# Kernel tuning notes

Hardware: AMD Instinct MI355X
Metric: run time of the kernel (lower is better)

The kernel has to match this reference:

```python
import jax, jax.numpy as jnp
import numpy as np

N = 16384      # nodes
E = 524288     # edges (avg degree 32)
D = 128        # node_dim
H = 256        # hidden_dim
C = 10         # num_classes
G = 64         # graphs in batch


def setup_inputs() -> dict:
    key = jax.random.key(0)
    ks = jax.random.split(key, 8)
    x = jax.random.normal(ks[0], (N, D), dtype=jnp.float32)
    edge_index = jax.random.randint(ks[1], (2, E), 0, N)
    batch = jnp.sort(jax.random.randint(ks[2], (N,), 0, G))
    s = 0.05
    W1 = jax.random.normal(ks[3], (D, H), dtype=jnp.float32) * s
    b1 = jnp.zeros((H,), dtype=jnp.float32)
    W2 = jax.random.normal(ks[4], (H, H), dtype=jnp.float32) * s
    b2 = jnp.zeros((H,), dtype=jnp.float32)
    Wc = jax.random.normal(ks[5], (H, C), dtype=jnp.float32) * s
    bc = jnp.zeros((C,), dtype=jnp.float32)
    return {"x": x, "edge_index": edge_index, "batch": batch,
            "W1": W1, "b1": b1, "W2": W2, "b2": b2, "Wc": Wc, "bc": bc}


def _adj_norm(edge_index, n, dtype):
    # dense adjacency with self-loops (duplicates collapse to 1 via .set),
    # symmetric degree normalization D^{-1/2} A D^{-1/2}
    adj = jnp.zeros((n, n), dtype=dtype)
    adj = adj.at[edge_index[0], edge_index[1]].set(1.0)
    diag = jnp.arange(n)
    adj = adj.at[diag, diag].set(1.0)
    deg = jnp.clip(adj.sum(axis=1), 1.0, None)
    dis = deg ** -0.5
    return dis[:, None] * adj * dis[None, :]


def reference(x, edge_index, batch, W1, b1, W2, b2, Wc, bc):
    n = x.shape[0]
    A = _adj_norm(edge_index, n, x.dtype)   # [n, n], same for both layers
    h = jax.nn.relu((A @ x) @ W1 + b1)      # GCN layer 1 + relu
    h = jax.nn.relu((A @ h) @ W2 + b2)      # GCN layer 2 + relu
    pooled = jax.ops.segment_sum(h, batch, num_segments=G)            # [G, H]
    counts = jax.ops.segment_sum(jnp.ones((n,), h.dtype), batch, num_segments=G)
    pooled = pooled / jnp.clip(counts, 1.0, None)[:, None]
    # dropout is identity in eval mode
    return pooled @ Wc + bc                  # [G, C]
```

## Files before the change

### kernel.cpp

```cpp
#include <hip/hip_runtime.h>
#include <hip/hip_fp16.h>

#define NN 16384
#define EE 524288
#define DDIM 128
#define HDIM 256
#define CDIM 10
#define GG 64
#define MAXD 128

typedef _Float16 h8 __attribute__((ext_vector_type(8)));
typedef float f4 __attribute__((ext_vector_type(4)));
typedef unsigned short su8 __attribute__((ext_vector_type(8)));

#define OFF_XH   0ull
#define OFF_ELL  4194304ull
#define OFF_ELLP 8388608ull
#define OFF_Y1H  16777216ull
#define OFF_H1   20971520ull
#define OFF_Y2H  29360128ull
#define OFF_DEG  37748736ull
#define OFF_DIS  37814272ull
#define OFF_POOL 37879808ull
#define OFF_CNT  37945344ull
#define OFF_WT1  37949440ull
#define OFF_WT2  38014976ull

__global__ void init_all(const float* __restrict__ x, _Float16* __restrict__ xh,
                         const float* __restrict__ W1, _Float16* __restrict__ wt1,
                         const float* __restrict__ W2, _Float16* __restrict__ wt2,
                         const int* __restrict__ ei, unsigned short* __restrict__ ell,
                         int* __restrict__ deg,
                         float* __restrict__ pooled, float* __restrict__ cnt,
                         const int* __restrict__ batch) {
    int b = blockIdx.x, t = threadIdx.x;
    if (b < 2048) {
        int i = (b * 256 + t) * 4;
        float4 v = *(const float4*)(x + i);
        _Float16 o[4] = {(_Float16)v.x, (_Float16)v.y, (_Float16)v.z, (_Float16)v.w};
        *(ushort4*)(xh + i) = *(ushort4*)o;
    } else if (b < 2176) {
        int i = (b - 2048) * 256 + t;
        int n = i / DDIM, k = i - n * DDIM;
        wt1[i] = (_Float16)W1[k * 256 + n];
    } else if (b < 2432) {
        int i = (b - 2176) * 256 + t;
        int n = i / HDIM, k = i - n * HDIM;
        wt2[i] = (_Float16)W2[k * 256 + n];
    } else if (b < 2496) {
        int r = (b - 2432) * 256 + t;
        pooled[r] = 0.0f;
        if (r < GG) {
            int lo = 0, hi = NN;
            while (lo < hi) { int m = (lo + hi) >> 1; if (batch[m] < r) lo = m + 1; else hi = m; }
            int a = lo;
            lo = 0; hi = NN;
            while (lo < hi) { int m = (lo + hi) >> 1; if (batch[m] < r + 1) lo = m + 1; else hi = m; }
            cnt[r] = (float)(lo - a);
        }
    } else {
        int e = ((b - 2496) * 256 + t) * 2;
        int2 s2 = *(const int2*)(ei + e);
        int2 d2 = *(const int2*)(ei + EE + e);
        int pos = atomicAdd(&deg[s2.x], 1) + 1;
        if (pos < MAXD) ell[s2.x * MAXD + pos] = (unsigned short)d2.x;
        pos = atomicAdd(&deg[s2.y], 1) + 1;
        if (pos < MAXD) ell[s2.y * MAXD + pos] = (unsigned short)d2.y;
    }
}

__global__ __launch_bounds__(256) void dedup_kernel(unsigned short* __restrict__ ell,
                                                    int* __restrict__ deg,
                                                    float* __restrict__ dis) {
    __shared__ unsigned bm[4][NN / 32];
    const int w = threadIdx.x >> 6, lane = threadIdx.x & 63;
    const int row = blockIdx.x * 4 + w;
    for (int i = lane; i < NN / 32; i += 64) bm[w][i] = 0u;
    __syncthreads();
    const int draw = deg[row] + 1;
    const int dl = (draw > MAXD) ? MAXD : draw;
    const size_t base = (size_t)row * MAXD;
    const int c0 = (lane == 0) ? row : (ell[base + lane] & (NN - 1));
    const int c1 = ell[base + 64 + lane] & (NN - 1);
    const bool v0 = lane < dl;
    const bool v1 = (64 + lane) < dl;
    bool k0 = false, k1 = false;
    if (v0) k0 = ((atomicOr(&bm[w][c0 >> 5], 1u << (c0 & 31)) >> (c0 & 31)) & 1u) == 0u;
    if (v1) k1 = ((atomicOr(&bm[w][c1 >> 5], 1u << (c1 & 31)) >> (c1 & 31)) & 1u) == 0u;
    const int u = __popcll(__ballot(k0)) + __popcll(__ballot(k1));
    if (lane == 0)
        ell[base] = (unsigned short)(row | (k0 ? 0 : 0x8000));
    else if (v0 && !k0)
        ell[base + lane] = (unsigned short)(c0 | 0x8000);
    if (v1 && !k1)
        ell[base + 64 + lane] = (unsigned short)(c1 | 0x8000);
    if (lane == 0) {
        deg[row] = dl;
        dis[row] = 1.0f / sqrtf((float)u);
    }
}

template <int COLS>
__global__ __launch_bounds__(256) void spmm_f16(const _Float16* __restrict__ src,
                                                const unsigned short* __restrict__ ell,
                                                const int* __restrict__ deg,
                                                const float* __restrict__ dis,
                                                _Float16* __restrict__ y) {
    constexpr int SEG = COLS / 8;
    constexpr int NS  = 64 / SEG;
    __shared__ unsigned scw[4][MAXD];
    const int t    = threadIdx.x;
    const int w    = t >> 6;
    const int lane = t & 63;
    const int row  = blockIdx.x * 4 + w;
    const size_t base = (size_t)row * MAXD;
    {
        unsigned r0 = ell[base + lane];
        unsigned r1 = ell[base + 64 + lane];
        int ca = r0 & (NN - 1), cb = r1 & (NN - 1);
        float wa = (r0 & 0x8000u) ? 0.0f : dis[ca];
        float wb = (r1 & 0x8000u) ? 0.0f : dis[cb];
        _Float16 ha = (_Float16)wa, hb = (_Float16)wb;
        scw[w][lane]      = (unsigned)ca | ((unsigned)(*(unsigned short*)&ha) << 16);
        scw[w][64 + lane] = (unsigned)cb | ((unsigned)(*(unsigned short*)&hb) << 16);
    }
    __syncthreads();
    const int d = deg[row];
    const float drow = dis[row];
    const int sid = lane / SEG;
    const int l   = lane % SEG;

    float acc[8];
#pragma unroll
    for (int j = 0; j < 8; j++) acc[j] = 0.0f;

#pragma unroll 4
    for (int k = sid; k < d; k += NS) {
        unsigned u = scw[w][k];
        int col = u & 0xFFFF;
        unsigned short wb = (unsigned short)(u >> 16);
        float wgt = (float)(*(_Float16*)&wb);
        su8 hv = *(const su8*)(src + (size_t)col * COLS + l * 8);
#pragma unroll
        for (int j = 0; j < 8; j++) {
            unsigned short hb = hv[j];
            acc[j] = fmaf(wgt, (float)(*(_Float16*)&hb), acc[j]);
        }
    }
#pragma unroll
    for (int off = SEG; off < 64; off <<= 1)
#pragma unroll
        for (int j = 0; j < 8; j++) acc[j] += __shfl_xor(acc[j], off, 64);

    if (lane < SEG) {
        su8 o;
#pragma unroll
        for (int j = 0; j < 8; j++) {
            _Float16 hv = (_Float16)(drow * acc[j]);
            o[j] = *(unsigned short*)&hv;
        }
        *(su8*)(y + (size_t)row * COLS + lane * 8) = o;
    }
}

#define ASTR 40
#define BSTR 40

#define MFMA_PROLOG                                                            \
    const int r0 = blockIdx.x * 128;                                           \
    const int c0 = blockIdx.y * 64;                                            \
    const int t = threadIdx.x;                                                 \
    const int lane = t & 63, wv = t >> 6;                                      \
    const int wm = wv >> 1, wn = wv & 1;                                       \
    const int qm = lane & 15, qk = lane >> 4;                                  \
    f4 acc[4][2];                                                              \
    _Pragma("unroll") for (int i = 0; i < 4; i++)                              \
        _Pragma("unroll") for (int j = 0; j < 2; j++)                          \
            acc[i][j] = (f4){0.f, 0.f, 0.f, 0.f};

#define MFMA_KLOOP(Aptr, Wtptr, K)                                             \
    for (int k0 = 0; k0 < K; k0 += 32) {                                       \
        __syncthreads();                                                       \
        {                                                                      \
            int r = t >> 1, ko = (t & 1) * 16;                                 \
            const su8* srcA = (const su8*)(Aptr + (size_t)(r0 + r) * K + k0 + ko); \
            su8 a0 = srcA[0], a1 = srcA[1];                                    \
            *(su8*)&As[r * ASTR + ko]     = a0;                                \
            *(su8*)&As[r * ASTR + ko + 8] = a1;                                \
            int n = t >> 2, ko2 = (t & 3) * 8;                                 \
            *(su8*)&Bs[n * BSTR + ko2] =                                       \
                *(const su8*)(Wtptr + (size_t)(c0 + n) * K + k0 + ko2);        \
        }                                                                      \
        __syncthreads();                                                       \
        h8 bfr[2];                                                             \
        _Pragma("unroll") for (int j = 0; j < 2; j++)                          \
            bfr[j] = *(const h8*)&Bs[(wn * 32 + j * 16 + qm) * BSTR + qk * 8]; \
        _Pragma("unroll") for (int i = 0; i < 4; i++) {                        \
            h8 afr = *(const h8*)&As[(wm * 64 + i * 16 + qm) * ASTR + qk * 8]; \
            _Pragma("unroll") for (int j = 0; j < 2; j++)                      \
                acc[i][j] = __builtin_amdgcn_mfma_f32_16x16x32_f16(            \
                    afr, bfr[j], acc[i][j], 0, 0, 0);                          \
        }                                                                      \
    }

template <int K>
__global__ __launch_bounds__(256) void gemm_mfma_f16(
        const _Float16* __restrict__ A, const _Float16* __restrict__ Wt,
        const float* __restrict__ bias, _Float16* __restrict__ H) {
    __shared__ __align__(16) _Float16 As[128 * ASTR];
    __shared__ __align__(16) _Float16 Bs[64 * BSTR];
    __shared__ __align__(16) _Float16 Cs[128 * 72];
    MFMA_PROLOG
    MFMA_KLOOP(A, Wt, K)

    float bv[2];
#pragma unroll
    for (int j = 0; j < 2; j++) bv[j] = bias[c0 + wn * 32 + j * 16 + qm];
#pragma unroll
    for (int i = 0; i < 4; i++)
#pragma unroll
        for (int j = 0; j < 2; j++) {
            int lc = wn * 32 + j * 16 + qm;
#pragma unroll
            for (int rr = 0; rr < 4; rr++) {
                int lr = wm * 64 + i * 16 + qk * 4 + rr;
                Cs[lr * 72 + lc] = (_Float16)fmaxf(acc[i][j][rr] + bv[j], 0.0f);
            }
        }
    __syncthreads();
    {
        int r = t >> 1, half_ = t & 1;
        _Float16* dst = H + (size_t)(r0 + r) * 256 + c0 + half_ * 32;
        const _Float16* srcc = &Cs[r * 72 + half_ * 32];
#pragma unroll
        for (int q = 0; q < 4; q++)
            *(su8*)(dst + q * 8) = *(const su8*)(srcc + q * 8);
    }
}

#define NG 8
template <int K>
__global__ __launch_bounds__(256) void gemm_mfma_pool(
        const _Float16* __restrict__ A, const _Float16* __restrict__ Wt,
        const float* __restrict__ bias, const int* __restrict__ batch,
        float* __restrict__ pooled) {
    __shared__ __align__(16) _Float16 As[128 * ASTR];
    __shared__ __align__(16) _Float16 Bs[64 * BSTR];
    __shared__ float pools[NG][68];
    __shared__ int sb[128];
    MFMA_PROLOG
    if (t < 128) sb[t] = batch[r0 + t];
    for (int i = t; i < NG * 68; i += 256) ((float*)pools)[i] = 0.0f;
    MFMA_KLOOP(A, Wt, K)

    float bv[2];
#pragma unroll
    for (int j = 0; j < 2; j++) bv[j] = bias[c0 + wn * 32 + j * 16 + qm];
    __syncthreads();
    const int g0 = sb[0];
#pragma unroll
    for (int i = 0; i < 4; i++)
#pragma unroll
        for (int j = 0; j < 2; j++) {
            int lc = wn * 32 + j * 16 + qm;
#pragma unroll
            for (int rr = 0; rr < 4; rr++) {
                int lr = wm * 64 + i * 16 + qk * 4 + rr;
                int gi = min(sb[lr] - g0, NG - 1);
                float v = fmaxf(acc[i][j][rr] + bv[j], 0.0f);
                atomicAdd(&pools[gi][lc], v);
            }
        }
    __syncthreads();
    const int ng = min(sb[127] - g0 + 1, NG);
    for (int i2 = t; i2 < ng * 64; i2 += 256) {
        int gi = i2 >> 6, c = i2 & 63;
        float v = pools[gi][c];
        if (v != 0.0f) atomicAdd(&pooled[(g0 + gi) * 256 + c0 + c], v);
    }
}

__global__ void head_kernel(const float* __restrict__ pooled,
                            const float* __restrict__ cnt,
                            const float* __restrict__ Wc,
                            const float* __restrict__ bc,
                            float* __restrict__ out) {
    int g = blockIdx.x;
    int l = threadIdx.x;
    float inv = 1.0f / fmaxf(cnt[g], 1.0f);
    float acc[CDIM];
#pragma unroll
    for (int c = 0; c < CDIM; c++) acc[c] = 0.0f;
    for (int t = l; t < 256; t += 64) {
        float pv = pooled[g * 256 + t] * inv;
#pragma unroll
        for (int c = 0; c < CDIM; c++) acc[c] = fmaf(pv, Wc[t * CDIM + c], acc[c]);
    }
#pragma unroll
    for (int c = 0; c < CDIM; c++) {
        float v = acc[c];
        for (int off = 32; off > 0; off >>= 1) v += __shfl_down(v, off, 64);
        if (l == 0) out[g * CDIM + c] = v + bc[c];
    }
}

extern "C" void kernel_launch(void* const* d_in, const int* in_sizes, int n_in,
                              void* d_out, int out_size, void* d_ws, size_t ws_size,
                              hipStream_t stream) {
    const float* x  = (const float*)d_in[0];
    const int*   ei = (const int*)d_in[1];
    const int*   batch = (const int*)d_in[2];
    const float* W1 = (const float*)d_in[3];
    const float* b1 = (const float*)d_in[4];
    const float* W2 = (const float*)d_in[5];
    const float* b2 = (const float*)d_in[6];
    const float* Wc = (const float*)d_in[7];
    const float* bc = (const float*)d_in[8];
    float* out = (float*)d_out;

    char* ws = (char*)d_ws;
    _Float16* xh   = (_Float16*)(ws + OFF_XH);
    unsigned short* ell = (unsigned short*)(ws + OFF_ELL);
    _Float16* y1h  = (_Float16*)(ws + OFF_Y1H);
    _Float16* h1   = (_Float16*)(ws + OFF_H1);
    _Float16* y2h  = (_Float16*)(ws + OFF_Y2H);
    int*   deg     = (int*)(ws + OFF_DEG);
    float* dis     = (float*)(ws + OFF_DIS);
    float* pooled  = (float*)(ws + OFF_POOL);
    float* cnt     = (float*)(ws + OFF_CNT);
    _Float16* wt1  = (_Float16*)(ws + OFF_WT1);
    _Float16* wt2  = (_Float16*)(ws + OFF_WT2);

    hipMemsetAsync(deg, 0, NN * sizeof(int), stream);
    init_all<<<3520, 256, 0, stream>>>(x, xh, W1, wt1, W2, wt2, ei, ell, deg,
                                       pooled, cnt, batch);
    dedup_kernel<<<NN / 4, 256, 0, stream>>>(ell, deg, dis);
    spmm_f16<DDIM><<<NN / 4, 256, 0, stream>>>(xh, ell, deg, dis, y1h);
    {
        dim3 grid(NN / 128, 256 / 64);
        gemm_mfma_f16<DDIM><<<grid, 256, 0, stream>>>(y1h, wt1, b1, h1);
    }
    spmm_f16<HDIM><<<NN / 4, 256, 0, stream>>>(h1, ell, deg, dis, y2h);
    {
        dim3 grid(NN / 128, 256 / 64);
        gemm_mfma_pool<HDIM><<<grid, 256, 0, stream>>>(y2h, wt2, b2, batch, pooled);
    }
    head_kernel<<<GG, 64, 0, stream>>>(pooled, cnt, Wc, bc, out);
}
```

Measured before the change: 185.5 us.

## Build adjacency via global dense bitmap instead of ELL append plus dedup

```diff
diff --git a/kernel.cpp b/kernel.cpp
--- a/kernel.cpp
+++ b/kernel.cpp
@@ -15,7 +15,6 @@
 
 #define OFF_XH   0ull
 #define OFF_ELL  4194304ull
-#define OFF_ELLP 8388608ull
 #define OFF_Y1H  16777216ull
 #define OFF_H1   20971520ull
 #define OFF_Y2H  29360128ull
@@ -25,12 +24,12 @@
 #define OFF_CNT  37945344ull
 #define OFF_WT1  37949440ull
 #define OFF_WT2  38014976ull
+#define OFF_BM   41943040ull
 
 __global__ void init_all(const float* __restrict__ x, _Float16* __restrict__ xh,
                          const float* __restrict__ W1, _Float16* __restrict__ wt1,
                          const float* __restrict__ W2, _Float16* __restrict__ wt2,
-                         const int* __restrict__ ei, unsigned short* __restrict__ ell,
-                         int* __restrict__ deg,
+                         const int* __restrict__ ei, unsigned* __restrict__ bitmap,
                          float* __restrict__ pooled, float* __restrict__ cnt,
                          const int* __restrict__ batch) {
     int b = blockIdx.x, t = threadIdx.x;
@@ -50,6 +49,7 @@
     } else if (b < 2496) {
         int r = (b - 2432) * 256 + t;
         pooled[r] = 0.0f;
+        atomicOr(&bitmap[(size_t)r * 512 + (r >> 5)], 1u << (r & 31));
         if (r < GG) {
             int lo = 0, hi = NN;
             while (lo < hi) { int m = (lo + hi) >> 1; if (batch[m] < r) lo = m + 1; else hi = m; }
@@ -62,41 +62,47 @@
         int e = ((b - 2496) * 256 + t) * 2;
         int2 s2 = *(const int2*)(ei + e);
         int2 d2 = *(const int2*)(ei + EE + e);
-        int pos = atomicAdd(&deg[s2.x], 1) + 1;
-        if (pos < MAXD) ell[s2.x * MAXD + pos] = (unsigned short)d2.x;
-        pos = atomicAdd(&deg[s2.y], 1) + 1;
-        if (pos < MAXD) ell[s2.y * MAXD + pos] = (unsigned short)d2.y;
-    }
-}
-
-__global__ __launch_bounds__(256) void dedup_kernel(unsigned short* __restrict__ ell,
-                                                    int* __restrict__ deg,
-                                                    float* __restrict__ dis) {
-    __shared__ unsigned bm[4][NN / 32];
+        atomicOr(&bitmap[(size_t)s2.x * 512 + (d2.x >> 5)], 1u << (d2.x & 31));
+        atomicOr(&bitmap[(size_t)s2.y * 512 + (d2.y >> 5)], 1u << (d2.y & 31));
+    }
+}
+
+__global__ __launch_bounds__(256) void extract_kernel(const unsigned* __restrict__ bitmap,
+                                                      unsigned short* __restrict__ ell,
+                                                      int* __restrict__ deg,
+                                                      float* __restrict__ dis) {
     const int w = threadIdx.x >> 6, lane = threadIdx.x & 63;
     const int row = blockIdx.x * 4 + w;
-    for (int i = lane; i < NN / 32; i += 64) bm[w][i] = 0u;
-    __syncthreads();
-    const int draw = deg[row] + 1;
-    const int dl = (draw > MAXD) ? MAXD : draw;
-    const size_t base = (size_t)row * MAXD;
-    const int c0 = (lane == 0) ? row : (ell[base + lane] & (NN - 1));
-    const int c1 = ell[base + 64 + lane] & (NN - 1);
-    const bool v0 = lane < dl;
-    const bool v1 = (64 + lane) < dl;
-    bool k0 = false, k1 = false;
-    if (v0) k0 = ((atomicOr(&bm[w][c0 >> 5], 1u << (c0 & 31)) >> (c0 & 31)) & 1u) == 0u;
-    if (v1) k1 = ((atomicOr(&bm[w][c1 >> 5], 1u << (c1 & 31)) >> (c1 & 31)) & 1u) == 0u;
-    const int u = __popcll(__ballot(k0)) + __popcll(__ballot(k1));
-    if (lane == 0)
-        ell[base] = (unsigned short)(row | (k0 ? 0 : 0x8000));
-    else if (v0 && !k0)
-        ell[base + lane] = (unsigned short)(c0 | 0x8000);
-    if (v1 && !k1)
-        ell[base + 64 + lane] = (unsigned short)(c1 | 0x8000);
-    if (lane == 0) {
-        deg[row] = dl;
-        dis[row] = 1.0f / sqrtf((float)u);
+    const uint4* bmr4 = (const uint4*)(bitmap + (size_t)row * 512);
+    uint4 A = bmr4[lane];
+    uint4 B = bmr4[lane + 64];
+    unsigned wds[8] = {A.x, A.y, A.z, A.w, B.x, B.y, B.z, B.w};
+    int cnt = 0;
+#pragma unroll
+    for (int i = 0; i < 8; i++) cnt += __popc(wds[i]);
+    int inc = cnt;
+#pragma unroll
+    for (int o = 1; o < 64; o <<= 1) {
+        int v = __shfl_up(inc, o, 64);
+        if (lane >= o) inc += v;
+    }
+    int p = inc - cnt;
+    const int total = __shfl(inc, 63, 64);
+    unsigned short* er = ell + (size_t)row * MAXD;
+#pragma unroll
+    for (int i = 0; i < 8; i++) {
+        unsigned m = wds[i];
+        int cbase = (i < 4) ? (lane * 128 + i * 32) : (8192 + lane * 128 + (i - 4) * 32);
+        while (m) {
+            int bb = __builtin_ctz(m);
+            m &= m - 1;
+            if (p < MAXD) er[p] = (unsigned short)(cbase + bb);
+            p++;
+        }
+    }
+    if (lane == 63) {
+        deg[row] = (total > MAXD) ? MAXD : total;
+        dis[row] = 1.0f / sqrtf((float)total);
     }
 }
 
@@ -115,12 +121,9 @@
     const int row  = blockIdx.x * 4 + w;
     const size_t base = (size_t)row * MAXD;
     {
-        unsigned r0 = ell[base + lane];
-        unsigned r1 = ell[base + 64 + lane];
-        int ca = r0 & (NN - 1), cb = r1 & (NN - 1);
-        float wa = (r0 & 0x8000u) ? 0.0f : dis[ca];
-        float wb = (r1 & 0x8000u) ? 0.0f : dis[cb];
-        _Float16 ha = (_Float16)wa, hb = (_Float16)wb;
+        int ca = ell[base + lane] & (NN - 1);
+        int cb = ell[base + 64 + lane] & (NN - 1);
+        _Float16 ha = (_Float16)dis[ca], hb = (_Float16)dis[cb];
         scw[w][lane]      = (unsigned)ca | ((unsigned)(*(unsigned short*)&ha) << 16);
         scw[w][64 + lane] = (unsigned)cb | ((unsigned)(*(unsigned short*)&hb) << 16);
     }
@@ -330,11 +333,12 @@
     float* cnt     = (float*)(ws + OFF_CNT);
     _Float16* wt1  = (_Float16*)(ws + OFF_WT1);
     _Float16* wt2  = (_Float16*)(ws + OFF_WT2);
-
-    hipMemsetAsync(deg, 0, NN * sizeof(int), stream);
-    init_all<<<3520, 256, 0, stream>>>(x, xh, W1, wt1, W2, wt2, ei, ell, deg,
+    unsigned* bitmap = (unsigned*)(ws + OFF_BM);
+
+    hipMemsetAsync(bitmap, 0, (size_t)NN * 512 * sizeof(unsigned), stream);
+    init_all<<<3520, 256, 0, stream>>>(x, xh, W1, wt1, W2, wt2, ei, bitmap,
                                        pooled, cnt, batch);
-    dedup_kernel<<<NN / 4, 256, 0, stream>>>(ell, deg, dis);
+    extract_kernel<<<NN / 4, 256, 0, stream>>>(bitmap, ell, deg, dis);
     spmm_f16<DDIM><<<NN / 4, 256, 0, stream>>>(xh, ell, deg, dis, y1h);
     {
         dim3 grid(NN / 128, 256 / 64);
```

Measured after the change: 196.2 us. 1.06x slower.

## Split ELL build into four partitioned degree counters and compact dedup output

Applied to the files above, without the earlier changes.

```diff
diff --git a/kernel.cpp b/kernel.cpp
--- a/kernel.cpp
+++ b/kernel.cpp
@@ -15,7 +15,7 @@
 
 #define OFF_XH   0ull
 #define OFF_ELL  4194304ull
-#define OFF_ELLP 8388608ull
+#define OFF_DEG4 8388608ull
 #define OFF_Y1H  16777216ull
 #define OFF_H1   20971520ull
 #define OFF_Y2H  29360128ull
@@ -30,25 +30,37 @@
                          const float* __restrict__ W1, _Float16* __restrict__ wt1,
                          const float* __restrict__ W2, _Float16* __restrict__ wt2,
                          const int* __restrict__ ei, unsigned short* __restrict__ ell,
-                         int* __restrict__ deg,
+                         int* __restrict__ deg4,
                          float* __restrict__ pooled, float* __restrict__ cnt,
                          const int* __restrict__ batch) {
     int b = blockIdx.x, t = threadIdx.x;
-    if (b < 2048) {
-        int i = (b * 256 + t) * 4;
+    if (b < 1024) {
+        int e = (b * 256 + t) * 2;
+        int2 s2 = *(const int2*)(ei + e);
+        int2 d2 = *(const int2*)(ei + EE + e);
+        int pa = e & 3;
+        int pb = (e + 1) & 3;
+        int capa = (pa == 3) ? 31 : 32;
+        int capb = (pb == 3) ? 31 : 32;
+        int pos = atomicAdd(&deg4[pa * NN + s2.x], 1);
+        if (pos < capa) ell[s2.x * MAXD + 1 + 32 * pa + pos] = (unsigned short)d2.x;
+        pos = atomicAdd(&deg4[pb * NN + s2.y], 1);
+        if (pos < capb) ell[s2.y * MAXD + 1 + 32 * pb + pos] = (unsigned short)d2.y;
+    } else if (b < 3072) {
+        int i = ((b - 1024) * 256 + t) * 4;
         float4 v = *(const float4*)(x + i);
         _Float16 o[4] = {(_Float16)v.x, (_Float16)v.y, (_Float16)v.z, (_Float16)v.w};
         *(ushort4*)(xh + i) = *(ushort4*)o;
-    } else if (b < 2176) {
-        int i = (b - 2048) * 256 + t;
+    } else if (b < 3200) {
+        int i = (b - 3072) * 256 + t;
         int n = i / DDIM, k = i - n * DDIM;
         wt1[i] = (_Float16)W1[k * 256 + n];
-    } else if (b < 2432) {
-        int i = (b - 2176) * 256 + t;
+    } else if (b < 3456) {
+        int i = (b - 3200) * 256 + t;
         int n = i / HDIM, k = i - n * HDIM;
         wt2[i] = (_Float16)W2[k * 256 + n];
-    } else if (b < 2496) {
-        int r = (b - 2432) * 256 + t;
+    } else {
+        int r = (b - 3456) * 256 + t;
         pooled[r] = 0.0f;
         if (r < GG) {
             int lo = 0, hi = NN;
@@ -58,18 +70,11 @@
             while (lo < hi) { int m = (lo + hi) >> 1; if (batch[m] < r + 1) lo = m + 1; else hi = m; }
             cnt[r] = (float)(lo - a);
         }
-    } else {
-        int e = ((b - 2496) * 256 + t) * 2;
-        int2 s2 = *(const int2*)(ei + e);
-        int2 d2 = *(const int2*)(ei + EE + e);
-        int pos = atomicAdd(&deg[s2.x], 1) + 1;
-        if (pos < MAXD) ell[s2.x * MAXD + pos] = (unsigned short)d2.x;
-        pos = atomicAdd(&deg[s2.y], 1) + 1;
-        if (pos < MAXD) ell[s2.y * MAXD + pos] = (unsigned short)d2.y;
     }
 }
 
 __global__ __launch_bounds__(256) void dedup_kernel(unsigned short* __restrict__ ell,
+                                                    const int* __restrict__ deg4,
                                                     int* __restrict__ deg,
                                                     float* __restrict__ dis) {
     __shared__ unsigned bm[4][NN / 32];
@@ -77,26 +82,40 @@
     const int row = blockIdx.x * 4 + w;
     for (int i = lane; i < NN / 32; i += 64) bm[w][i] = 0u;
     __syncthreads();
-    const int draw = deg[row] + 1;
-    const int dl = (draw > MAXD) ? MAXD : draw;
+    const int cp0 = min(deg4[row], 32);
+    const int cp1 = min(deg4[NN + row], 32);
+    const int cp2 = min(deg4[2 * NN + row], 32);
+    const int cp3 = min(deg4[3 * NN + row], 31);
     const size_t base = (size_t)row * MAXD;
     const int c0 = (lane == 0) ? row : (ell[base + lane] & (NN - 1));
     const int c1 = ell[base + 64 + lane] & (NN - 1);
-    const bool v0 = lane < dl;
-    const bool v1 = (64 + lane) < dl;
+    bool v0, v1;
+    if (lane == 0) v0 = true;
+    else {
+        int p = (lane - 1) >> 5, o = (lane - 1) & 31;
+        int c = (p == 0) ? cp0 : cp1;
+        v0 = o < c;
+    }
+    {
+        int j = 63 + lane;
+        int p = j >> 5, o = j & 31;
+        int c = (p == 1) ? cp1 : (p == 2) ? cp2 : cp3;
+        v1 = o < c;
+    }
     bool k0 = false, k1 = false;
     if (v0) k0 = ((atomicOr(&bm[w][c0 >> 5], 1u << (c0 & 31)) >> (c0 & 31)) & 1u) == 0u;
     if (v1) k1 = ((atomicOr(&bm[w][c1 >> 5], 1u << (c1 & 31)) >> (c1 & 31)) & 1u) == 0u;
-    const int u = __popcll(__ballot(k0)) + __popcll(__ballot(k1));
-    if (lane == 0)
-        ell[base] = (unsigned short)(row | (k0 ? 0 : 0x8000));
-    else if (v0 && !k0)
-        ell[base + lane] = (unsigned short)(c0 | 0x8000);
-    if (v1 && !k1)
-        ell[base + 64 + lane] = (unsigned short)(c1 | 0x8000);
+    unsigned long long m0 = __ballot(k0);
+    unsigned long long m1 = __ballot(k1);
+    const int nd = __popcll(m0) + __popcll(m1);
+    unsigned long long below = (lane == 0) ? 0ull : ((~0ull) >> (64 - lane));
+    int p0 = __popcll(m0 & below);
+    int p1 = __popcll(m0) + __popcll(m1 & below);
+    if (k0) ell[base + p0] = (unsigned short)c0;
+    if (k1) ell[base + p1] = (unsigned short)c1;
     if (lane == 0) {
-        deg[row] = dl;
-        dis[row] = 1.0f / sqrtf((float)u);
+        deg[row] = nd;
+        dis[row] = 1.0f / sqrtf((float)nd);
     }
 }
 
@@ -115,12 +134,9 @@
     const int row  = blockIdx.x * 4 + w;
     const size_t base = (size_t)row * MAXD;
     {
-        unsigned r0 = ell[base + lane];
-        unsigned r1 = ell[base + 64 + lane];
-        int ca = r0 & (NN - 1), cb = r1 & (NN - 1);
-        float wa = (r0 & 0x8000u) ? 0.0f : dis[ca];
-        float wb = (r1 & 0x8000u) ? 0.0f : dis[cb];
-        _Float16 ha = (_Float16)wa, hb = (_Float16)wb;
+        int ca = ell[base + lane] & (NN - 1);
+        int cb = ell[base + 64 + lane] & (NN - 1);
+        _Float16 ha = (_Float16)dis[ca], hb = (_Float16)dis[cb];
         scw[w][lane]      = (unsigned)ca | ((unsigned)(*(unsigned short*)&ha) << 16);
         scw[w][64 + lane] = (unsigned)cb | ((unsigned)(*(unsigned short*)&hb) << 16);
     }
@@ -321,6 +337,7 @@
     char* ws = (char*)d_ws;
     _Float16* xh   = (_Float16*)(ws + OFF_XH);
     unsigned short* ell = (unsigned short*)(ws + OFF_ELL);
+    int*   deg4    = (int*)(ws + OFF_DEG4);
     _Float16* y1h  = (_Float16*)(ws + OFF_Y1H);
     _Float16* h1   = (_Float16*)(ws + OFF_H1);
     _Float16* y2h  = (_Float16*)(ws + OFF_Y2H);
@@ -331,10 +348,10 @@
     _Float16* wt1  = (_Float16*)(ws + OFF_WT1);
     _Float16* wt2  = (_Float16*)(ws + OFF_WT2);
 
-    hipMemsetAsync(deg, 0, NN * sizeof(int), stream);
-    init_all<<<3520, 256, 0, stream>>>(x, xh, W1, wt1, W2, wt2, ei, ell, deg,
+    hipMemsetAsync(deg4, 0, 4 * NN * sizeof(int), stream);
+    init_all<<<3520, 256, 0, stream>>>(x, xh, W1, wt1, W2, wt2, ei, ell, deg4,
                                        pooled, cnt, batch);
-    dedup_kernel<<<NN / 4, 256, 0, stream>>>(ell, deg, dis);
+    dedup_kernel<<<NN / 4, 256, 0, stream>>>(ell, deg4, deg, dis);
     spmm_f16<DDIM><<<NN / 4, 256, 0, stream>>>(xh, ell, deg, dis, y1h);
     {
         dim3 grid(NN / 128, 256 / 64);
```

New measurement: 195.3 us. 5.3% more time.
